# Performance work log

Measured on AMD Instinct MI355X. Metric: run time of the kernel, lower is better.

## Reference

```python
import jax, jax.numpy as jnp
import numpy as np

DIM = 128
HEADS = 4
HEAD_DIM = DIM // HEADS
SCALE = HEAD_DIM ** -0.5


def setup_inputs() -> dict:
    k0 = jax.random.key(0)
    ks = jax.random.split(k0, 20)
    B, N, Hq, Wq_, Hk, Wk_ = 1, 6, 100, 100, 16, 44
    s = 0.02
    return {
        "query": jax.random.normal(ks[0], (B, DIM, Hq, Wq_), jnp.float32),
        "key": jax.random.normal(ks[1], (B, N, DIM, Hk, Wk_), jnp.float32),
        "value": jax.random.normal(ks[2], (B, N, DIM, Hk, Wk_), jnp.float32),
        "depth": jax.random.uniform(ks[3], (B, N, 1, Hk, Wk_), jnp.float32),
        "depth_confidence": jax.random.uniform(ks[4], (B, N, 1, Hk, Wk_), jnp.float32),
        "skip": jax.random.normal(ks[5], (B, DIM, Hq, Wq_), jnp.float32),
        "Wq": jax.random.normal(ks[6], (DIM, DIM), jnp.float32) * s,
        "bq": jnp.zeros((DIM,), jnp.float32),
        "Wk": jax.random.normal(ks[7], (DIM, DIM), jnp.float32) * s,
        "bk": jnp.zeros((DIM,), jnp.float32),
        "Wv": jax.random.normal(ks[8], (DIM, DIM), jnp.float32) * s,
        "bv": jnp.zeros((DIM,), jnp.float32),
        "Wo": jax.random.normal(ks[9], (DIM, DIM), jnp.float32) * s,
        "bo": jnp.zeros((DIM,), jnp.float32),
        "dw1": jax.random.normal(ks[10], (DIM // 4, 1), jnp.float32) * s,  # 1x1 conv: 1 -> dim/4
        "db1": jnp.zeros((DIM // 4,), jnp.float32),
        "dw2": jax.random.normal(ks[11], (HEADS, DIM // 4), jnp.float32) * s,  # 1x1 conv: dim/4 -> heads
        "db2": jnp.zeros((HEADS,), jnp.float32),
    }


def _forward(query, key, value, depth, depth_confidence, skip,
             Wq, bq, Wk, bk, Wv, bv, Wo, bo, dw1, db1, dw2, db2):
    B, dim, Hq, Wq_ = query.shape
    N, Hk, Wk_ = key.shape[1], key.shape[3], key.shape[4]
    Lq, Lk = Hq * Wq_, N * Hk * Wk_

    # b d h w -> b (h w) d
    qf = jnp.transpose(query, (0, 2, 3, 1)).reshape(B, Lq, dim)
    # b n d h w -> b (n h w) d
    kf = jnp.transpose(key, (0, 1, 3, 4, 2)).reshape(B, Lk, dim)
    vf = jnp.transpose(value, (0, 1, 3, 4, 2)).reshape(B, Lk, dim)

    def heads(x, W, b):  # (B,L,dim) -> (B,H,L,hd)
        y = x @ W.T + b
        return jnp.transpose(y.reshape(B, -1, HEADS, HEAD_DIM), (0, 2, 1, 3))

    Q = heads(qf, Wq, bq)
    K = heads(kf, Wk, bk)
    V = heads(vf, Wv, bv)

    attn = jnp.einsum('bhqd,bhkd->bhqk', Q, K) * SCALE  # (B,H,Lq,Lk)

    # depth weighting bias: two 1x1 convs + softmax over heads channel
    d = jnp.transpose(depth, (0, 1, 3, 4, 2))  # (B,N,Hk,Wk,1)
    t = jax.nn.relu(d @ dw1.T + db1)            # (B,N,Hk,Wk,dim/4)
    t = t @ dw2.T + db2                          # (B,N,Hk,Wk,heads)
    dw = jax.nn.softmax(t, axis=-1)
    conf = jnp.transpose(depth_confidence, (0, 1, 3, 4, 2))  # (B,N,Hk,Wk,1)
    cw = conf * dw                               # (B,N,Hk,Wk,heads)
    bias = 0.1 * jnp.transpose(cw, (0, 4, 1, 2, 3)).reshape(B, HEADS, 1, Lk)

    attn = jax.nn.softmax(attn + bias, axis=-1)
    out = jnp.einsum('bhqk,bhkd->bhqd', attn, V)             # (B,H,Lq,hd)
    out = jnp.transpose(out, (0, 2, 1, 3)).reshape(B, Lq, dim)
    out = out @ Wo.T + bo
    out = jnp.transpose(out.reshape(B, Hq, Wq_, dim), (0, 3, 1, 2))
    return out + skip


def reference(query, key, value, depth, depth_confidence, skip,
              Wq, bq, Wk, bk, Wv, bv, Wo, bo, dw1, db1, dw2, db2):
    return _forward(query, key, value, depth, depth_confidence, skip,
                    Wq, bq, Wk, bk, Wv, bv, Wo, bo, dw1, db1, dw2, db2)
```

## Files before the change

### kernel.cpp

```cpp
#include <hip/hip_runtime.h>
#include <stdint.h>

#define LQ 10000
#define LK 4224
#define NQB 313
#define SCALE 0.17677669529663687f

typedef __bf16 bf16x8 __attribute__((ext_vector_type(8)));
typedef float  f32x4  __attribute__((ext_vector_type(4)));
typedef unsigned short u16x4 __attribute__((ext_vector_type(4)));

__device__ __forceinline__ unsigned short f2b(float f) {
  union { float f; unsigned u; } v; v.f = f;
  unsigned r = v.u + 0x7fffu + ((v.u >> 16) & 1u);
  return (unsigned short)(r >> 16);
}

__global__ void misc_kernel(
    const float* __restrict__ depth, const float* __restrict__ conf,
    const float* __restrict__ dw1, const float* __restrict__ db1,
    const float* __restrict__ dw2, const float* __restrict__ db2,
    const float* __restrict__ Wq, const float* __restrict__ Wk,
    const float* __restrict__ Wv, const float* __restrict__ Wo,
    float* __restrict__ biasArr,
    unsigned short* __restrict__ Wqb, unsigned short* __restrict__ Wkb,
    unsigned short* __restrict__ Wvb, unsigned short* __restrict__ Wob) {
  int b = blockIdx.x, t = threadIdx.x;
  if (b < 256) {
    int i = b * 256 + t;
    int m = i >> 14, j = i & 16383;
    const float* src = (m == 0) ? Wq : (m == 1) ? Wk : (m == 2) ? Wv : Wo;
    unsigned short* dst = (m == 0) ? Wqb : (m == 1) ? Wkb : (m == 2) ? Wvb : Wob;
    dst[j] = f2b(src[j]);
    return;
  }
  int k = (b - 256) * 256 + t;
  if (k >= LK) return;
  float d = depth[k], c = conf[k];
  float t2[4];
#pragma unroll
  for (int hh = 0; hh < 4; ++hh) t2[hh] = db2[hh];
  for (int cc = 0; cc < 32; ++cc) {
    float t1 = fmaxf(fmaf(d, dw1[cc], db1[cc]), 0.f);
#pragma unroll
    for (int hh = 0; hh < 4; ++hh) t2[hh] = fmaf(t1, dw2[hh * 32 + cc], t2[hh]);
  }
  float mx = fmaxf(fmaxf(t2[0], t2[1]), fmaxf(t2[2], t2[3]));
  float e[4], s = 0.f;
#pragma unroll
  for (int hh = 0; hh < 4; ++hh) { e[hh] = __expf(t2[hh] - mx); s += e[hh]; }
  float f = 0.1f * c / s;
#pragma unroll
  for (int hh = 0; hh < 4; ++hh) biasArr[hh * LK + k] = f * e[hh];
}

__global__ __launch_bounds__(256) void proj_q_kernel(
    const float* __restrict__ X, const unsigned short* __restrict__ Wb,
    const float* __restrict__ bias, unsigned short* __restrict__ Y) {
  __shared__ __align__(16) unsigned short Xb[64][136];
  int t = threadIdx.x;
  int l0 = blockIdx.x * 64;
#pragma unroll
  for (int i = 0; i < 32; ++i) {
    int e = t + 256 * i;
    int d = e >> 6, c = e & 63;
    int l = l0 + c;
    Xb[c][d] = f2b(l < LQ ? X[(size_t)d * LQ + l] : 0.f);
  }
  __syncthreads();
  int wv = t >> 6, lane = t & 63, lm = lane & 15, lg = lane >> 4;
  const f32x4 zf = {0.f, 0.f, 0.f, 0.f};
  bf16x8 af[4];
#pragma unroll
  for (int kk = 0; kk < 4; ++kk)
    af[kk] = *(const bf16x8*)&Xb[wv * 16 + lm][kk * 32 + lg * 8];
  f32x4 acc[8] = {zf, zf, zf, zf, zf, zf, zf, zf};
#pragma unroll
  for (int kk = 0; kk < 4; ++kk)
#pragma unroll
    for (int ni = 0; ni < 8; ++ni) {
      bf16x8 bfr = *(const bf16x8*)(Wb + (size_t)(ni * 16 + lm) * 128 + kk * 32 + lg * 8);
      acc[ni] = __builtin_amdgcn_mfma_f32_16x16x32_bf16(af[kk], bfr, acc[ni], 0, 0, 0);
    }
#pragma unroll
  for (int ni = 0; ni < 8; ++ni)
#pragma unroll
    for (int r = 0; r < 4; ++r) {
      int l = l0 + wv * 16 + lg * 4 + r;
      int dout = ni * 16 + lm;
      Y[(size_t)l * 128 + dout] = f2b(acc[ni][r] + bias[dout]);
    }
}

__global__ __launch_bounds__(256) void proj_kv_kernel(
    const float* __restrict__ key, const float* __restrict__ value,
    const unsigned short* __restrict__ Wkb, const float* __restrict__ bk,
    const unsigned short* __restrict__ Wvb, const float* __restrict__ bv,
    unsigned short* __restrict__ Kb, unsigned short* __restrict__ Vt) {
  __shared__ __align__(16) unsigned short Xb[64][136];
  int t = threadIdx.x;
  int isV = blockIdx.y;
  const float* X = isV ? value : key;
  const unsigned short* Wb = isV ? Wvb : Wkb;
  const float* bb = isV ? bv : bk;
  int k0 = blockIdx.x * 64;
  int n = k0 / 704, p0 = k0 % 704;
  const float* Xn = X + (size_t)n * 128 * 704 + p0;
#pragma unroll
  for (int i = 0; i < 32; ++i) {
    int e = t + 256 * i;
    int d = e >> 6, c = e & 63;
    Xb[c][d] = f2b(Xn[(size_t)d * 704 + c]);
  }
  __syncthreads();
  int wv = t >> 6, lane = t & 63, lm = lane & 15, lg = lane >> 4;
  const f32x4 zf = {0.f, 0.f, 0.f, 0.f};
  bf16x8 af[4];
#pragma unroll
  for (int kk = 0; kk < 4; ++kk)
    af[kk] = *(const bf16x8*)&Xb[wv * 16 + lm][kk * 32 + lg * 8];
  f32x4 acc[8] = {zf, zf, zf, zf, zf, zf, zf, zf};
#pragma unroll
  for (int kk = 0; kk < 4; ++kk)
#pragma unroll
    for (int ni = 0; ni < 8; ++ni) {
      bf16x8 bfr = *(const bf16x8*)(Wb + (size_t)(ni * 16 + lm) * 128 + kk * 32 + lg * 8);
      acc[ni] = __builtin_amdgcn_mfma_f32_16x16x32_bf16(af[kk], bfr, acc[ni], 0, 0, 0);
    }
  if (!isV) {
#pragma unroll
    for (int ni = 0; ni < 8; ++ni)
#pragma unroll
      for (int r = 0; r < 4; ++r) {
        int k = k0 + wv * 16 + lg * 4 + r;
        int dout = ni * 16 + lm;
        Kb[(size_t)k * 128 + dout] = f2b(acc[ni][r] + bb[dout]);
      }
  } else {
#pragma unroll
    for (int ni = 0; ni < 8; ++ni)
#pragma unroll
      for (int r = 0; r < 4; ++r) {
        int k = k0 + wv * 16 + lg * 4 + r;
        int dout = ni * 16 + lm;
        Vt[(size_t)dout * LK + k] = f2b(acc[ni][r] + bb[dout]);
      }
  }
}

__global__ __launch_bounds__(256) void attn_part_kernel(
    const unsigned short* __restrict__ Qb, const unsigned short* __restrict__ Kb,
    const unsigned short* __restrict__ Vt, const float* __restrict__ biasArr,
    float* __restrict__ Opart, float* __restrict__ Ml, int tpc, int C) {
  __shared__ __align__(16) unsigned short P_lds[4][32][72];
  int t = threadIdx.x;
  int wv = t >> 6;
  int qb = blockIdx.x * 4 + wv;
  if (qb >= NQB) return;
  int h = blockIdx.y, c = blockIdx.z;
  int lane = t & 63, lm = lane & 15, lg = lane >> 4;
  const f32x4 zf = {0.f, 0.f, 0.f, 0.f};

  bf16x8 qf[2];
#pragma unroll
  for (int mi = 0; mi < 2; ++mi)
    qf[mi] = *(const bf16x8*)(Qb + (size_t)(qb * 32 + mi * 16 + lm) * 128 + h * 32 + lg * 8);

  f32x4 acc[2][2] = {{zf, zf}, {zf, zf}};
  float mrun[2][4], lrun[2][4];
#pragma unroll
  for (int mi = 0; mi < 2; ++mi)
#pragma unroll
    for (int r = 0; r < 4; ++r) { mrun[mi][r] = -1e30f; lrun[mi][r] = 0.f; }

  const float* bias_h = biasArr + h * LK;
  const unsigned short* Kh = Kb + h * 32;
  const unsigned short* Vh = Vt + (size_t)h * 32 * LK;

  int kb_end = c * tpc + tpc;
  for (int kb = c * tpc; kb < kb_end; ++kb) {
    int k0 = kb * 64;
    bf16x8 kf[4];
#pragma unroll
    for (int ni = 0; ni < 4; ++ni)
      kf[ni] = *(const bf16x8*)(Kh + (size_t)(k0 + ni * 16 + lm) * 128 + lg * 8);
    f32x4 S[2][4];
#pragma unroll
    for (int mi = 0; mi < 2; ++mi)
#pragma unroll
      for (int ni = 0; ni < 4; ++ni)
        S[mi][ni] = __builtin_amdgcn_mfma_f32_16x16x32_bf16(qf[mi], kf[ni], zf, 0, 0, 0);
    float bvv[4];
#pragma unroll
    for (int ni = 0; ni < 4; ++ni) bvv[ni] = bias_h[k0 + ni * 16 + lm];

#pragma unroll
    for (int mi = 0; mi < 2; ++mi) {
      float sv[4][4], rmax[4], rsum[4], fac[4];
#pragma unroll
      for (int r = 0; r < 4; ++r) rmax[r] = -1e30f;
#pragma unroll
      for (int ni = 0; ni < 4; ++ni)
#pragma unroll
        for (int r = 0; r < 4; ++r) {
          float x = fmaf(S[mi][ni][r], SCALE, bvv[ni]);
          sv[ni][r] = x;
          rmax[r] = fmaxf(rmax[r], x);
        }
#pragma unroll
      for (int r = 0; r < 4; ++r) {
#pragma unroll
        for (int msk = 1; msk < 16; msk <<= 1)
          rmax[r] = fmaxf(rmax[r], __shfl_xor(rmax[r], msk));
        float mn = fmaxf(mrun[mi][r], rmax[r]);
        fac[r] = __expf(mrun[mi][r] - mn);
        mrun[mi][r] = mn;
        rsum[r] = 0.f;
      }
#pragma unroll
      for (int ni = 0; ni < 4; ++ni)
#pragma unroll
        for (int r = 0; r < 4; ++r) {
          float p = __expf(sv[ni][r] - mrun[mi][r]);
          sv[ni][r] = p;
          rsum[r] += p;
        }
#pragma unroll
      for (int r = 0; r < 4; ++r) {
#pragma unroll
        for (int msk = 1; msk < 16; msk <<= 1)
          rsum[r] += __shfl_xor(rsum[r], msk);
        lrun[mi][r] = fmaf(lrun[mi][r], fac[r], rsum[r]);
      }
#pragma unroll
      for (int nd = 0; nd < 2; ++nd)
#pragma unroll
        for (int r = 0; r < 4; ++r) acc[mi][nd][r] *= fac[r];
#pragma unroll
      for (int ni = 0; ni < 4; ++ni)
#pragma unroll
        for (int r = 0; r < 4; ++r)
          P_lds[wv][mi * 16 + lg * 4 + r][ni * 16 + lm] = f2b(sv[ni][r]);
    }
    __builtin_amdgcn_sched_barrier(0);
    bf16x8 pa[2][2], vfr[2][2];
#pragma unroll
    for (int mi = 0; mi < 2; ++mi)
#pragma unroll
      for (int kk = 0; kk < 2; ++kk)
        pa[mi][kk] = *(const bf16x8*)&P_lds[wv][mi * 16 + lm][kk * 32 + lg * 8];
#pragma unroll
    for (int kk = 0; kk < 2; ++kk)
#pragma unroll
      for (int nd = 0; nd < 2; ++nd)
        vfr[kk][nd] = *(const bf16x8*)(Vh + (size_t)(nd * 16 + lm) * LK + k0 + kk * 32 + lg * 8);
#pragma unroll
    for (int mi = 0; mi < 2; ++mi)
#pragma unroll
      for (int nd = 0; nd < 2; ++nd)
#pragma unroll
        for (int kk = 0; kk < 2; ++kk)
          acc[mi][nd] = __builtin_amdgcn_mfma_f32_16x16x32_bf16(pa[mi][kk], vfr[kk][nd], acc[mi][nd], 0, 0, 0);
    __builtin_amdgcn_sched_barrier(0);
  }
  size_t pbase = (size_t)(qb * 4 + h) * C + c;
  float* Op = Opart + pbase * 1024;
#pragma unroll
  for (int mi = 0; mi < 2; ++mi)
#pragma unroll
    for (int nd = 0; nd < 2; ++nd)
#pragma unroll
      for (int r = 0; r < 4; ++r)
        Op[(mi * 16 + lg * 4 + r) * 32 + nd * 16 + lm] = acc[mi][nd][r];
  if (lm == 0) {
    float* MlB = Ml + pbase * 64;
#pragma unroll
    for (int mi = 0; mi < 2; ++mi)
#pragma unroll
      for (int r = 0; r < 4; ++r) {
        MlB[mi * 16 + lg * 4 + r] = mrun[mi][r];
        MlB[32 + mi * 16 + lg * 4 + r] = lrun[mi][r];
      }
  }
}

__global__ __launch_bounds__(256) void combine_kernel(
    const float* __restrict__ Opart, const float* __restrict__ Ml,
    unsigned short* __restrict__ Ob, int C) {
  __shared__ float wls[4][7][32];
  int t = threadIdx.x, wv = t >> 6, lane = t & 63;
  int qb = blockIdx.x * 4 + wv;
  if (qb >= NQB) return;
  int h = blockIdx.y;
  size_t base = (size_t)(qb * 4 + h) * C;
  if (lane < 32) {
    float M = -1e30f;
    for (int c = 0; c < C; ++c)
      M = fmaxf(M, Ml[(base + c) * 64 + lane]);
    float lt = 0.f;
    for (int c = 0; c < C; ++c) {
      float w = __expf(Ml[(base + c) * 64 + lane] - M);
      wls[wv][c][lane] = w;
      lt += Ml[(base + c) * 64 + 32 + lane] * w;
    }
    wls[wv][6][lane] = 1.f / lt;
  }
  __builtin_amdgcn_sched_barrier(0);
  const float* Op = Opart + base * 1024;
#pragma unroll
  for (int j = 0; j < 4; ++j) {
    int q = j * 8 + (lane >> 3);
    int d = (lane & 7) * 4;
    f32x4 accv = {0.f, 0.f, 0.f, 0.f};
    for (int c = 0; c < C; ++c) {
      f32x4 v = *(const f32x4*)(Op + c * 1024 + j * 256 + lane * 4);
      float w = wls[wv][c][q];
#pragma unroll
      for (int i = 0; i < 4; ++i) accv[i] = fmaf(v[i], w, accv[i]);
    }
    float linv = wls[wv][6][q];
    u16x4 o4;
#pragma unroll
    for (int i = 0; i < 4; ++i) o4[i] = f2b(accv[i] * linv);
    *(u16x4*)(Ob + (size_t)(qb * 32 + q) * 128 + h * 32 + d) = o4;
  }
}

__global__ __launch_bounds__(256) void epi_kernel(
    const unsigned short* __restrict__ Ob, const unsigned short* __restrict__ Wob,
    const float* __restrict__ bo, const float* __restrict__ skip,
    float* __restrict__ out) {
  int t = threadIdx.x, wv = t >> 6, lane = t & 63, lm = lane & 15, lg = lane >> 4;
  int l0 = blockIdx.x * 64;
  const f32x4 zf = {0.f, 0.f, 0.f, 0.f};
  bf16x8 af[2][4];
#pragma unroll
  for (int mi = 0; mi < 2; ++mi)
#pragma unroll
    for (int kk = 0; kk < 4; ++kk)
      af[mi][kk] = *(const bf16x8*)(Wob + (size_t)(wv * 32 + mi * 16 + lm) * 128 + kk * 32 + lg * 8);
  f32x4 acc[2][4] = {{zf, zf, zf, zf}, {zf, zf, zf, zf}};
#pragma unroll
  for (int kk = 0; kk < 4; ++kk) {
    bf16x8 bfr[4];
#pragma unroll
    for (int ni = 0; ni < 4; ++ni)
      bfr[ni] = *(const bf16x8*)(Ob + (size_t)(l0 + ni * 16 + lm) * 128 + kk * 32 + lg * 8);
#pragma unroll
    for (int mi = 0; mi < 2; ++mi)
#pragma unroll
      for (int ni = 0; ni < 4; ++ni)
        acc[mi][ni] = __builtin_amdgcn_mfma_f32_16x16x32_bf16(af[mi][kk], bfr[ni], acc[mi][ni], 0, 0, 0);
  }
#pragma unroll
  for (int mi = 0; mi < 2; ++mi)
#pragma unroll
    for (int r = 0; r < 4; ++r) {
      int dout = wv * 32 + mi * 16 + lg * 4 + r;
      float bb = bo[dout];
#pragma unroll
      for (int ni = 0; ni < 4; ++ni) {
        int l = l0 + ni * 16 + lm;
        if (l < LQ)
          out[(size_t)dout * LQ + l] = acc[mi][ni][r] + bb + skip[(size_t)dout * LQ + l];
      }
    }
}

extern "C" void kernel_launch(void* const* d_in, const int* in_sizes, int n_in,
                              void* d_out, int out_size, void* d_ws, size_t ws_size,
                              hipStream_t stream) {
  const float* query = (const float*)d_in[0];
  const float* key   = (const float*)d_in[1];
  const float* value = (const float*)d_in[2];
  const float* depth = (const float*)d_in[3];
  const float* conf  = (const float*)d_in[4];
  const float* skip  = (const float*)d_in[5];
  const float* Wq = (const float*)d_in[6];   const float* bq = (const float*)d_in[7];
  const float* Wk = (const float*)d_in[8];   const float* bk = (const float*)d_in[9];
  const float* Wv = (const float*)d_in[10];  const float* bv = (const float*)d_in[11];
  const float* Wo = (const float*)d_in[12];  const float* bo = (const float*)d_in[13];
  const float* dw1 = (const float*)d_in[14]; const float* db1 = (const float*)d_in[15];
  const float* dw2 = (const float*)d_in[16]; const float* db2 = (const float*)d_in[17];
  float* out = (float*)d_out;
  char* ws = (char*)d_ws;

  unsigned short* Qb   = (unsigned short*)(ws + 0);
  unsigned short* Kb   = (unsigned short*)(ws + 2572288);
  unsigned short* Vt   = (unsigned short*)(ws + 3653632);
  float*          bias = (float*)        (ws + 4734976);
  unsigned short* Wqb  = (unsigned short*)(ws + 4802560);
  unsigned short* Wkb  = (unsigned short*)(ws + 4835328);
  unsigned short* Wvb  = (unsigned short*)(ws + 4868096);
  unsigned short* Wob  = (unsigned short*)(ws + 4900864);
  unsigned short* Ob   = (unsigned short*)(ws + 4933632);
  const size_t splitOff = 7505920;

  int C = 1;
  {
    const int cand[4] = {6, 3, 2, 1};
    for (int i = 0; i < 4; ++i) {
      size_t need = splitOff + (size_t)NQB * 4 * cand[i] * (4096 + 256);
      if (ws_size >= need) { C = cand[i]; break; }
    }
  }
  int tpc = 66 / C;
  float* Opart = (float*)(ws + splitOff);
  float* Ml    = (float*)(ws + splitOff + (size_t)NQB * 4 * C * 4096);

  hipLaunchKernelGGL(misc_kernel, dim3(273), dim3(256), 0, stream,
                     depth, conf, dw1, db1, dw2, db2, Wq, Wk, Wv, Wo,
                     bias, Wqb, Wkb, Wvb, Wob);
  hipLaunchKernelGGL(proj_q_kernel, dim3(157), dim3(256), 0, stream,
                     query, Wqb, bq, Qb);
  hipLaunchKernelGGL(proj_kv_kernel, dim3(66, 2), dim3(256), 0, stream,
                     key, value, Wkb, bk, Wvb, bv, Kb, Vt);
  hipLaunchKernelGGL(attn_part_kernel, dim3(79, 4, C), dim3(256), 0, stream,
                     Qb, Kb, Vt, bias, Opart, Ml, tpc, C);
  hipLaunchKernelGGL(combine_kernel, dim3(79, 4), dim3(256), 0, stream,
                     Opart, Ml, Ob, C);
  hipLaunchKernelGGL(epi_kernel, dim3(157), dim3(256), 0, stream,
                     Ob, Wob, bo, skip, out);
}
```

Baseline: 276.1 us.

## Compute transposed QK^T so softmax rows live per-lane, cutting shuffles

Swaps the MFMA operand order so the score tile is transposed: each lane now owns one query row's values across its four registers. Row max and sum need only two cross-group shuffles instead of four-step butterflies per register, and P is written to LDS as packed bf16x4 vectors instead of scalar stores. Bias is loaded as a float4, and the rescale factor is redistributed to the accumulator layout with four shuffles. Compiler memory barriers are added around the sched barriers to keep LDS ordering intact.

New measurement: 260.9 us. 1.06x faster.

```diff
diff --git a/kernel.cpp b/kernel.cpp
--- a/kernel.cpp
+++ b/kernel.cpp
@@ -7,6 +7,7 @@
 #define SCALE 0.17677669529663687f
 
 typedef __bf16 bf16x8 __attribute__((ext_vector_type(8)));
+typedef __bf16 bf16x4 __attribute__((ext_vector_type(4)));
 typedef float  f32x4  __attribute__((ext_vector_type(4)));
 typedef unsigned short u16x4 __attribute__((ext_vector_type(4)));
 
@@ -167,11 +168,7 @@
     qf[mi] = *(const bf16x8*)(Qb + (size_t)(qb * 32 + mi * 16 + lm) * 128 + h * 32 + lg * 8);
 
   f32x4 acc[2][2] = {{zf, zf}, {zf, zf}};
-  float mrun[2][4], lrun[2][4];
-#pragma unroll
-  for (int mi = 0; mi < 2; ++mi)
-#pragma unroll
-    for (int r = 0; r < 4; ++r) { mrun[mi][r] = -1e30f; lrun[mi][r] = 0.f; }
+  float mrun[2] = {-1e30f, -1e30f}, lrun[2] = {0.f, 0.f};
 
   const float* bias_h = biasArr + h * LK;
   const unsigned short* Kh = Kb + h * 32;
@@ -189,59 +186,52 @@
     for (int mi = 0; mi < 2; ++mi)
 #pragma unroll
       for (int ni = 0; ni < 4; ++ni)
-        S[mi][ni] = __builtin_amdgcn_mfma_f32_16x16x32_bf16(qf[mi], kf[ni], zf, 0, 0, 0);
-    float bvv[4];
-#pragma unroll
-    for (int ni = 0; ni < 4; ++ni) bvv[ni] = bias_h[k0 + ni * 16 + lm];
+        S[mi][ni] = __builtin_amdgcn_mfma_f32_16x16x32_bf16(kf[ni], qf[mi], zf, 0, 0, 0);
+    f32x4 bvv[4];
+#pragma unroll
+    for (int ni = 0; ni < 4; ++ni)
+      bvv[ni] = *(const f32x4*)(bias_h + k0 + ni * 16 + lg * 4);
 
 #pragma unroll
     for (int mi = 0; mi < 2; ++mi) {
-      float sv[4][4], rmax[4], rsum[4], fac[4];
-#pragma unroll
-      for (int r = 0; r < 4; ++r) rmax[r] = -1e30f;
+      float pmax = -1e30f;
 #pragma unroll
       for (int ni = 0; ni < 4; ++ni)
 #pragma unroll
         for (int r = 0; r < 4; ++r) {
-          float x = fmaf(S[mi][ni][r], SCALE, bvv[ni]);
-          sv[ni][r] = x;
-          rmax[r] = fmaxf(rmax[r], x);
+          float x = fmaf(S[mi][ni][r], SCALE, bvv[ni][r]);
+          S[mi][ni][r] = x;
+          pmax = fmaxf(pmax, x);
         }
-#pragma unroll
-      for (int r = 0; r < 4; ++r) {
-#pragma unroll
-        for (int msk = 1; msk < 16; msk <<= 1)
-          rmax[r] = fmaxf(rmax[r], __shfl_xor(rmax[r], msk));
-        float mn = fmaxf(mrun[mi][r], rmax[r]);
-        fac[r] = __expf(mrun[mi][r] - mn);
-        mrun[mi][r] = mn;
-        rsum[r] = 0.f;
+      pmax = fmaxf(pmax, __shfl_xor(pmax, 16));
+      pmax = fmaxf(pmax, __shfl_xor(pmax, 32));
+      float mn = fmaxf(mrun[mi], pmax);
+      float fac = __expf(mrun[mi] - mn);
+      mrun[mi] = mn;
+      float psum = 0.f;
+#pragma unroll
+      for (int ni = 0; ni < 4; ++ni) {
+        bf16x4 pk;
+#pragma unroll
+        for (int r = 0; r < 4; ++r) {
+          float p = __expf(S[mi][ni][r] - mn);
+          psum += p;
+          pk[r] = (__bf16)p;
+        }
+        *(bf16x4*)&P_lds[wv][mi * 16 + lm][ni * 16 + lg * 4] = pk;
       }
-#pragma unroll
-      for (int ni = 0; ni < 4; ++ni)
-#pragma unroll
-        for (int r = 0; r < 4; ++r) {
-          float p = __expf(sv[ni][r] - mrun[mi][r]);
-          sv[ni][r] = p;
-          rsum[r] += p;
-        }
-#pragma unroll
-      for (int r = 0; r < 4; ++r) {
-#pragma unroll
-        for (int msk = 1; msk < 16; msk <<= 1)
-          rsum[r] += __shfl_xor(rsum[r], msk);
-        lrun[mi][r] = fmaf(lrun[mi][r], fac[r], rsum[r]);
-      }
+      psum += __shfl_xor(psum, 16);
+      psum += __shfl_xor(psum, 32);
+      lrun[mi] = fmaf(lrun[mi], fac, psum);
+      float fac_t[4];
+#pragma unroll
+      for (int r = 0; r < 4; ++r) fac_t[r] = __shfl(fac, lg * 4 + r);
 #pragma unroll
       for (int nd = 0; nd < 2; ++nd)
 #pragma unroll
-        for (int r = 0; r < 4; ++r) acc[mi][nd][r] *= fac[r];
-#pragma unroll
-      for (int ni = 0; ni < 4; ++ni)
-#pragma unroll
-        for (int r = 0; r < 4; ++r)
-          P_lds[wv][mi * 16 + lg * 4 + r][ni * 16 + lm] = f2b(sv[ni][r]);
-    }
+        for (int r = 0; r < 4; ++r) acc[mi][nd][r] *= fac_t[r];
+    }
+    asm volatile("" ::: "memory");
     __builtin_amdgcn_sched_barrier(0);
     bf16x8 pa[2][2], vfr[2][2];
 #pragma unroll
@@ -261,6 +251,7 @@
 #pragma unroll
         for (int kk = 0; kk < 2; ++kk)
           acc[mi][nd] = __builtin_amdgcn_mfma_f32_16x16x32_bf16(pa[mi][kk], vfr[kk][nd], acc[mi][nd], 0, 0, 0);
+    asm volatile("" ::: "memory");
     __builtin_amdgcn_sched_barrier(0);
   }
   size_t pbase = (size_t)(qb * 4 + h) * C + c;
@@ -272,15 +263,13 @@
 #pragma unroll
       for (int r = 0; r < 4; ++r)
         Op[(mi * 16 + lg * 4 + r) * 32 + nd * 16 + lm] = acc[mi][nd][r];
-  if (lm == 0) {
+  if (lane < 16) {
     float* MlB = Ml + pbase * 64;
 #pragma unroll
-    for (int mi = 0; mi < 2; ++mi)
-#pragma unroll
-      for (int r = 0; r < 4; ++r) {
-        MlB[mi * 16 + lg * 4 + r] = mrun[mi][r];
-        MlB[32 + mi * 16 + lg * 4 + r] = lrun[mi][r];
-      }
+    for (int mi = 0; mi < 2; ++mi) {
+      MlB[mi * 16 + lm] = mrun[mi];
+      MlB[32 + mi * 16 + lm] = lrun[mi];
+    }
   }
 }
 
@@ -305,6 +294,7 @@
     }
     wls[wv][6][lane] = 1.f / lt;
   }
+  asm volatile("" ::: "memory");
   __builtin_amdgcn_sched_barrier(0);
   const float* Op = Opart + base * 1024;
 #pragma unroll
```
